# Performance work log

Hardware: AMD Instinct MI355X
Metric: run time of the kernel (lower is better)

Reference implementation:

```python
import jax, jax.numpy as jnp
import numpy as np


def setup_inputs() -> dict:
    key = jax.random.key(0)
    k1, k2 = jax.random.split(key)
    B, EMB, CODES, NUM_TOKENS = 16, 64, 16384, 1024
    x_in = jax.random.normal(k1, (B, EMB, CODES), dtype=jnp.float32)
    code_embedding = jax.random.uniform(k2, (NUM_TOKENS, EMB), dtype=jnp.float32)
    return {"x_in": x_in, "code_embedding": code_embedding}


def reference(x_in, code_embedding):
    # x_in: [B, emb, codes]; code_embedding: [num_tokens, emb]
    x_t = jnp.transpose(x_in, (0, 2, 1))  # [B, codes, emb]
    # squared euclidean distances (argmin is invariant to sqrt used by cdist)
    x2 = jnp.sum(x_t * x_t, axis=-1)                      # [B, codes]
    e2 = jnp.sum(code_embedding * code_embedding, axis=-1)  # [num_tokens]
    dots = jnp.einsum('bce,ke->bck', x_t, code_embedding)   # [B, codes, num_tokens]
    dist2 = x2[:, :, None] - 2.0 * dots + e2[None, None, :]
    indices = jnp.argmin(dist2, axis=2)                   # [B, codes]
    x_out = jnp.transpose(code_embedding[indices], (0, 2, 1))  # [B, emb, codes]
    return x_out, indices[:, :, None]  # indices keepdim like torch argmin(keepdim=True)
```

## Files before the change

### kernel.cpp

```cpp
#include <hip/hip_runtime.h>


#define BB 16
#define EMB 64
#define CODES 16384
#define NT 1024
#define NTILES 64
#define CHUNK 4
#define EPOCHS (NTILES / CHUNK)
#define QPB 256

typedef __attribute__((ext_vector_type(8))) short s16x8;
typedef __attribute__((ext_vector_type(4))) float f32x4;
typedef __attribute__((ext_vector_type(4))) int i32x4;
typedef unsigned int u32;

__device__ inline short bf16_hi(float f) { return (short)(__builtin_bit_cast(u32, f) >> 16); }
__device__ inline float hi_part(float f) { return __builtin_bit_cast(float, __builtin_bit_cast(u32, f) & 0xFFFF0000u); }
__device__ inline u32 umax_(u32 a, u32 b) { return a > b ? a : b; }

__device__ inline void async_copy16(const char* g, char* lds_base_uniform) {
  __builtin_amdgcn_global_load_lds(
      (const __attribute__((address_space(1))) unsigned int*)g,
      (__attribute__((address_space(3))) unsigned int*)(unsigned int)(unsigned long long)lds_base_uniform,
      16, 0, 0);
}

#define WSE_OFF   0
#define WSH_OFF   266240
#define WSH2_OFF  270336

__global__ __launch_bounds__(256) void vq_prep(const float* __restrict__ E,
                                               char* __restrict__ wsE,
                                               float* __restrict__ wsh,
                                               float* __restrict__ wsh2) {
  const int bid = blockIdx.x, tid = threadIdx.x;
  if (bid < 32) {
    const int gid = bid * 256 + tid;
    const int nt = gid >> 7, ks = (gid >> 6) & 1, lane = gid & 63;
    const int col = lane & 15, quad = lane >> 4;
    const int n = nt * 16 + col;
    const int k0 = ks * 32 + quad * 8;
    const float* ep = E + n * EMB + k0;
    s16x8 hv, lv;
    #pragma unroll
    for (int j = 0; j < 8; ++j) {
      float v = ep[j];
      float hf = hi_part(v);
      hv[j] = bf16_hi(v);
      lv[j] = bf16_hi(v - hf);
    }
    char* base = wsE + ((size_t)nt << 12) + ((size_t)ks << 10) + lane * 16;
    *(i32x4*)(base)        = __builtin_bit_cast(i32x4, hv);
    *(i32x4*)(base + 2048) = __builtin_bit_cast(i32x4, lv);
  } else {
    const int n = (bid - 32) * 256 + tid;
    if (n < NT) {
      const float4* ep = (const float4*)(E + n * EMB);
      float s = 0.f;
      #pragma unroll
      for (int g = 0; g < 16; ++g) { float4 v = ep[g]; s += v.x*v.x + v.y*v.y + v.z*v.z + v.w*v.w; }
      const float h = -0.5f * s;
      wsh[n] = h;
      wsh2[n] = 16384.f * (h + 128.f);
    }
  }
}

__global__ __launch_bounds__(512, 4) void vq_main(
    const float* __restrict__ x, const float* __restrict__ E,
    const char* __restrict__ wsE, const float* __restrict__ wsh,
    const float* __restrict__ wsh2,
    float* __restrict__ xout, float* __restrict__ iout) {
  __shared__ char smem[2 * CHUNK * 4096 + 4096];
  float* lh = (float*)(smem + 2 * CHUNK * 4096);
  const int tid = threadIdx.x;
  const int wave = tid >> 6, lane = tid & 63;
  const int col = lane & 15, quad = lane >> 4;
  const int b = blockIdx.y;
  const int c0 = blockIdx.x * QPB;
  const int cw = c0 + wave * 32;

  ((float2*)lh)[tid] = ((const float2*)wsh2)[tid];
  {
    const char* g = wsE + wave * 2048 + lane * 16;
    char* lb = smem + wave * 2048;
    async_copy16(g,        lb);
    async_copy16(g + 1024, lb + 1024);
  }

  s16x8 ah[2][2], al[2][2];
  #pragma unroll
  for (int mt = 0; mt < 2; ++mt) {
    #pragma unroll
    for (int ks = 0; ks < 2; ++ks) {
      s16x8 hv, lv;
      #pragma unroll
      for (int j = 0; j < 8; ++j) {
        const int e = ks * 32 + quad * 8 + j;
        float v = x[((size_t)b * EMB + e) * CODES + (size_t)(cw + mt * 16 + col)] * 16384.f;
        float hf = hi_part(v);
        hv[j] = bf16_hi(v);
        lv[j] = bf16_hi(v - hf);
      }
      ah[mt][ks] = hv;
      al[mt][ks] = lv;
    }
  }

  u32 k1[2][4], k2[2][4];
  #pragma unroll
  for (int mt = 0; mt < 2; ++mt)
    #pragma unroll
    for (int r = 0; r < 4; ++r) { k1[mt][r] = 0u; k2[mt][r] = 0u; }

  u32 inv = 1023u - (u32)col;

  __syncthreads();

  for (int c = 0; c < EPOCHS; ++c) {
    if (c < EPOCHS - 1) {
      const char* g = wsE + (size_t)(c + 1) * (CHUNK * 4096) + wave * 2048 + lane * 16;
      char* lb = smem + ((c + 1) & 1) * (CHUNK * 4096) + wave * 2048;
      async_copy16(g,        lb);
      async_copy16(g + 1024, lb + 1024);
    }

    const char* rb = smem + (c & 1) * (CHUNK * 4096) + lane * 16;
    #pragma unroll
    for (int t = 0; t < CHUNK; ++t) {
      const char* p = rb + t * 4096;
      const s16x8 bh0 = __builtin_bit_cast(s16x8, *(const i32x4*)(p));
      const s16x8 bh1 = __builtin_bit_cast(s16x8, *(const i32x4*)(p + 1024));
      const s16x8 bl0 = __builtin_bit_cast(s16x8, *(const i32x4*)(p + 2048));
      const s16x8 bl1 = __builtin_bit_cast(s16x8, *(const i32x4*)(p + 3072));
      const float ch = lh[(c * CHUNK + t) * 16 + col];
      const f32x4 cq = (f32x4){ch, ch, ch, ch};

      f32x4 acc[2];
      #pragma unroll
      for (int mt = 0; mt < 2; ++mt) {
        acc[mt] = __builtin_amdgcn_mfma_f32_16x16x32_bf16(ah[mt][0], bh0, cq, 0, 0, 0);
        acc[mt] = __builtin_amdgcn_mfma_f32_16x16x32_bf16(ah[mt][1], bh1, acc[mt], 0, 0, 0);
        acc[mt] = __builtin_amdgcn_mfma_f32_16x16x32_bf16(al[mt][0], bh0, acc[mt], 0, 0, 0);
        acc[mt] = __builtin_amdgcn_mfma_f32_16x16x32_bf16(al[mt][1], bh1, acc[mt], 0, 0, 0);
        acc[mt] = __builtin_amdgcn_mfma_f32_16x16x32_bf16(ah[mt][0], bl0, acc[mt], 0, 0, 0);
        acc[mt] = __builtin_amdgcn_mfma_f32_16x16x32_bf16(ah[mt][1], bl1, acc[mt], 0, 0, 0);
      }

      #pragma unroll
      for (int mt = 0; mt < 2; ++mt) {
        #pragma unroll
        for (int r = 0; r < 4; ++r) {
          u32 q = (u32)acc[mt][r];
          u32 key = (q << 10) + inv;
          u32 k1o = k1[mt][r];
          asm("v_med3_u32 %0, %1, %2, %3"
              : "=v"(k2[mt][r]) : "v"(key), "v"(k1o), "v"(k2[mt][r]));
          k1[mt][r] = umax_(key, k1o);
        }
      }
      inv -= 16u;
    }
    __syncthreads();
  }

  uint2* cand = (uint2*)smem;
  int* idxs = (int*)(smem + 2048);
  #pragma unroll
  for (int mt = 0; mt < 2; ++mt) {
    #pragma unroll
    for (int r = 0; r < 4; ++r) {
      u32 a1 = k1[mt][r], a2 = k2[mt][r];
      #pragma unroll
      for (int m = 1; m <= 8; m <<= 1) {
        u32 r1 = __shfl_xor(a1, m, 64);
        u32 r2 = __shfl_xor(a2, m, 64);
        u32 t = a1 < r1 ? a1 : r1;
        a1 = umax_(a1, r1);
        a2 = umax_(umax_(a2, r2), t);
      }
      if (col == r) cand[wave * 32 + mt * 16 + quad * 4 + r] = make_uint2(a1, a2);
    }
  }
  __syncthreads();

  if (tid < QPB) {
    const u32 K1 = cand[tid].x, K2 = cand[tid].y;
    const int i1 = 1023 - (int)(K1 & 1023u);
    const int i2 = 1023 - (int)(K2 & 1023u);
    const float* xq = x + (size_t)b * EMB * CODES + (size_t)(c0 + tid);
    const float4* e1 = (const float4*)(E + i1 * EMB);
    const float4* e2 = (const float4*)(E + i2 * EMB);
    float d10 = 0, d11 = 0, d12 = 0, d13 = 0, d20 = 0, d21 = 0, d22 = 0, d23 = 0;
    #pragma unroll
    for (int g = 0; g < 16; ++g) {
      float4 a = e1[g], c4 = e2[g];
      float x0 = xq[(size_t)(4 * g + 0) * CODES];
      float x1 = xq[(size_t)(4 * g + 1) * CODES];
      float x2 = xq[(size_t)(4 * g + 2) * CODES];
      float x3 = xq[(size_t)(4 * g + 3) * CODES];
      d10 = fmaf(x0, a.x, d10);  d11 = fmaf(x1, a.y, d11);
      d12 = fmaf(x2, a.z, d12);  d13 = fmaf(x3, a.w, d13);
      d20 = fmaf(x0, c4.x, d20); d21 = fmaf(x1, c4.y, d21);
      d22 = fmaf(x2, c4.z, d22); d23 = fmaf(x3, c4.w, d23);
    }
    const float s1 = ((d10 + d11) + (d12 + d13)) + wsh[i1];
    const float s2 = ((d20 + d21) + (d22 + d23)) + wsh[i2];
    const bool take2 = (s2 > s1) || (s2 == s1 && i2 < i1);
    const int idx = take2 ? i2 : i1;
    idxs[tid] = idx;
    iout[(size_t)b * CODES + (size_t)(c0 + tid)] = (float)idx;
  }
  __syncthreads();

  {
    const int q = tid & (QPB - 1);
    const int eh = (tid >> 8) * 32;
    const int idx = idxs[q];
    const float* Er = E + idx * EMB + eh;
    float* xo = xout + ((size_t)b * EMB + eh) * CODES + (size_t)(c0 + q);
    #pragma unroll
    for (int e = 0; e < 32; ++e) xo[(size_t)e * CODES] = Er[e];
  }
}

extern "C" void kernel_launch(void* const* d_in, const int* in_sizes, int n_in,
                              void* d_out, int out_size, void* d_ws, size_t ws_size,
                              hipStream_t stream) {
  const float* x = (const float*)d_in[0];
  const float* E = (const float*)d_in[1];
  float* xout = (float*)d_out;
  float* iout = (float*)d_out + (size_t)BB * EMB * CODES;

  char* wsE  = (char*)d_ws + WSE_OFF;
  float* wsh  = (float*)((char*)d_ws + WSH_OFF);
  float* wsh2 = (float*)((char*)d_ws + WSH2_OFF);

  vq_prep<<<36, 256, 0, stream>>>(E, wsE, wsh, wsh2);
  vq_main<<<dim3(CODES / QPB, BB), 512, 0, stream>>>(x, E, wsE, wsh, wsh2, xout, iout);
}
```

Before: 204.7 us.

## Double CHUNK, prefetch next LDS tile, split MFMA chains, parallelize rescoring

```diff
diff --git a/kernel.cpp b/kernel.cpp
--- a/kernel.cpp
+++ b/kernel.cpp
@@ -6,7 +6,7 @@
 #define CODES 16384
 #define NT 1024
 #define NTILES 64
-#define CHUNK 4
+#define CHUNK 8
 #define EPOCHS (NTILES / CHUNK)
 #define QPB 256
 
@@ -83,10 +83,12 @@
 
   ((float2*)lh)[tid] = ((const float2*)wsh2)[tid];
   {
-    const char* g = wsE + wave * 2048 + lane * 16;
-    char* lb = smem + wave * 2048;
+    const char* g = wsE + wave * 4096 + lane * 16;
+    char* lb = smem + wave * 4096;
     async_copy16(g,        lb);
     async_copy16(g + 1024, lb + 1024);
+    async_copy16(g + 2048, lb + 2048);
+    async_copy16(g + 3072, lb + 3072);
   }
 
   s16x8 ah[2][2], al[2][2];
@@ -120,39 +122,52 @@
 
   for (int c = 0; c < EPOCHS; ++c) {
     if (c < EPOCHS - 1) {
-      const char* g = wsE + (size_t)(c + 1) * (CHUNK * 4096) + wave * 2048 + lane * 16;
-      char* lb = smem + ((c + 1) & 1) * (CHUNK * 4096) + wave * 2048;
+      const char* g = wsE + (size_t)(c + 1) * (CHUNK * 4096) + wave * 4096 + lane * 16;
+      char* lb = smem + ((c + 1) & 1) * (CHUNK * 4096) + wave * 4096;
       async_copy16(g,        lb);
       async_copy16(g + 1024, lb + 1024);
+      async_copy16(g + 2048, lb + 2048);
+      async_copy16(g + 3072, lb + 3072);
     }
 
     const char* rb = smem + (c & 1) * (CHUNK * 4096) + lane * 16;
+    i32x4 fb0 = *(const i32x4*)(rb);
+    i32x4 fb1 = *(const i32x4*)(rb + 1024);
+    i32x4 fb2 = *(const i32x4*)(rb + 2048);
+    i32x4 fb3 = *(const i32x4*)(rb + 3072);
+    float ch = lh[(c * CHUNK) * 16 + col];
+
     #pragma unroll
     for (int t = 0; t < CHUNK; ++t) {
-      const char* p = rb + t * 4096;
-      const s16x8 bh0 = __builtin_bit_cast(s16x8, *(const i32x4*)(p));
-      const s16x8 bh1 = __builtin_bit_cast(s16x8, *(const i32x4*)(p + 1024));
-      const s16x8 bl0 = __builtin_bit_cast(s16x8, *(const i32x4*)(p + 2048));
-      const s16x8 bl1 = __builtin_bit_cast(s16x8, *(const i32x4*)(p + 3072));
-      const float ch = lh[(c * CHUNK + t) * 16 + col];
+      i32x4 nb0, nb1, nb2, nb3; float nch;
+      if (t < CHUNK - 1) {
+        const char* p = rb + (t + 1) * 4096;
+        nb0 = *(const i32x4*)(p);
+        nb1 = *(const i32x4*)(p + 1024);
+        nb2 = *(const i32x4*)(p + 2048);
+        nb3 = *(const i32x4*)(p + 3072);
+        nch = lh[(c * CHUNK + t + 1) * 16 + col];
+      }
+      const s16x8 bh0 = __builtin_bit_cast(s16x8, fb0);
+      const s16x8 bh1 = __builtin_bit_cast(s16x8, fb1);
+      const s16x8 bl0 = __builtin_bit_cast(s16x8, fb2);
+      const s16x8 bl1 = __builtin_bit_cast(s16x8, fb3);
       const f32x4 cq = (f32x4){ch, ch, ch, ch};
-
-      f32x4 acc[2];
+      const f32x4 zz = (f32x4){0.f, 0.f, 0.f, 0.f};
+
       #pragma unroll
       for (int mt = 0; mt < 2; ++mt) {
-        acc[mt] = __builtin_amdgcn_mfma_f32_16x16x32_bf16(ah[mt][0], bh0, cq, 0, 0, 0);
-        acc[mt] = __builtin_amdgcn_mfma_f32_16x16x32_bf16(ah[mt][1], bh1, acc[mt], 0, 0, 0);
-        acc[mt] = __builtin_amdgcn_mfma_f32_16x16x32_bf16(al[mt][0], bh0, acc[mt], 0, 0, 0);
-        acc[mt] = __builtin_amdgcn_mfma_f32_16x16x32_bf16(al[mt][1], bh1, acc[mt], 0, 0, 0);
-        acc[mt] = __builtin_amdgcn_mfma_f32_16x16x32_bf16(ah[mt][0], bl0, acc[mt], 0, 0, 0);
-        acc[mt] = __builtin_amdgcn_mfma_f32_16x16x32_bf16(ah[mt][1], bl1, acc[mt], 0, 0, 0);
-      }
-
-      #pragma unroll
-      for (int mt = 0; mt < 2; ++mt) {
+        f32x4 cA = __builtin_amdgcn_mfma_f32_16x16x32_bf16(ah[mt][0], bh0, cq, 0, 0, 0);
+        f32x4 cB = __builtin_amdgcn_mfma_f32_16x16x32_bf16(al[mt][1], bh1, zz, 0, 0, 0);
+        cA = __builtin_amdgcn_mfma_f32_16x16x32_bf16(ah[mt][1], bh1, cA, 0, 0, 0);
+        cB = __builtin_amdgcn_mfma_f32_16x16x32_bf16(ah[mt][0], bl0, cB, 0, 0, 0);
+        cA = __builtin_amdgcn_mfma_f32_16x16x32_bf16(al[mt][0], bh0, cA, 0, 0, 0);
+        cB = __builtin_amdgcn_mfma_f32_16x16x32_bf16(ah[mt][1], bl1, cB, 0, 0, 0);
+        const f32x4 a = cA + cB;
+
         #pragma unroll
         for (int r = 0; r < 4; ++r) {
-          u32 q = (u32)acc[mt][r];
+          u32 q = (u32)a[r];
           u32 key = (q << 10) + inv;
           u32 k1o = k1[mt][r];
           asm("v_med3_u32 %0, %1, %2, %3"
@@ -161,6 +176,7 @@
         }
       }
       inv -= 16u;
+      if (t < CHUNK - 1) { fb0 = nb0; fb1 = nb1; fb2 = nb2; fb3 = nb3; ch = nch; }
     }
     __syncthreads();
   }
@@ -185,32 +201,30 @@
   }
   __syncthreads();
 
-  if (tid < QPB) {
-    const u32 K1 = cand[tid].x, K2 = cand[tid].y;
-    const int i1 = 1023 - (int)(K1 & 1023u);
-    const int i2 = 1023 - (int)(K2 & 1023u);
-    const float* xq = x + (size_t)b * EMB * CODES + (size_t)(c0 + tid);
-    const float4* e1 = (const float4*)(E + i1 * EMB);
-    const float4* e2 = (const float4*)(E + i2 * EMB);
-    float d10 = 0, d11 = 0, d12 = 0, d13 = 0, d20 = 0, d21 = 0, d22 = 0, d23 = 0;
+  {
+    const int q = tid >> 1, which = tid & 1;
+    const u32 K = which ? cand[q].y : cand[q].x;
+    const int i = 1023 - (int)(K & 1023u);
+    const float* xq = x + (size_t)b * EMB * CODES + (size_t)(c0 + q);
+    const float4* ei = (const float4*)(E + i * EMB);
+    float d0 = 0, d1 = 0, d2 = 0, d3 = 0;
     #pragma unroll
     for (int g = 0; g < 16; ++g) {
-      float4 a = e1[g], c4 = e2[g];
-      float x0 = xq[(size_t)(4 * g + 0) * CODES];
-      float x1 = xq[(size_t)(4 * g + 1) * CODES];
-      float x2 = xq[(size_t)(4 * g + 2) * CODES];
-      float x3 = xq[(size_t)(4 * g + 3) * CODES];
-      d10 = fmaf(x0, a.x, d10);  d11 = fmaf(x1, a.y, d11);
-      d12 = fmaf(x2, a.z, d12);  d13 = fmaf(x3, a.w, d13);
-      d20 = fmaf(x0, c4.x, d20); d21 = fmaf(x1, c4.y, d21);
-      d22 = fmaf(x2, c4.z, d22); d23 = fmaf(x3, c4.w, d23);
-    }
-    const float s1 = ((d10 + d11) + (d12 + d13)) + wsh[i1];
-    const float s2 = ((d20 + d21) + (d22 + d23)) + wsh[i2];
-    const bool take2 = (s2 > s1) || (s2 == s1 && i2 < i1);
-    const int idx = take2 ? i2 : i1;
-    idxs[tid] = idx;
-    iout[(size_t)b * CODES + (size_t)(c0 + tid)] = (float)idx;
+      float4 a = ei[g];
+      d0 = fmaf(xq[(size_t)(4 * g + 0) * CODES], a.x, d0);
+      d1 = fmaf(xq[(size_t)(4 * g + 1) * CODES], a.y, d1);
+      d2 = fmaf(xq[(size_t)(4 * g + 2) * CODES], a.z, d2);
+      d3 = fmaf(xq[(size_t)(4 * g + 3) * CODES], a.w, d3);
+    }
+    const float s = ((d0 + d1) + (d2 + d3)) + wsh[i];
+    const float s_o = __shfl_xor(s, 1, 64);
+    const int i_o = __shfl_xor(i, 1, 64);
+    if (which == 0) {
+      const bool take2 = (s_o > s) || (s_o == s && i_o < i);
+      const int idx = take2 ? i_o : i;
+      idxs[q] = idx;
+      iout[(size_t)b * CODES + (size_t)(c0 + q)] = (float)idx;
+    }
   }
   __syncthreads();
 
```

Result: no change. 208.5 us (+1.8%).

## Switch distance GEMM to 32x32x16 MFMA with 256-thread blocks

Applied to the files above, without the earlier changes.

```diff
diff --git a/kernel.cpp b/kernel.cpp
--- a/kernel.cpp
+++ b/kernel.cpp
@@ -5,13 +5,14 @@
 #define EMB 64
 #define CODES 16384
 #define NT 1024
-#define NTILES 64
+#define NTILES 32
 #define CHUNK 4
 #define EPOCHS (NTILES / CHUNK)
 #define QPB 256
+#define TILE_B 8192
 
 typedef __attribute__((ext_vector_type(8))) short s16x8;
-typedef __attribute__((ext_vector_type(4))) float f32x4;
+typedef __attribute__((ext_vector_type(16))) float f32x16;
 typedef __attribute__((ext_vector_type(4))) int i32x4;
 typedef unsigned int u32;
 
@@ -37,11 +38,8 @@
   const int bid = blockIdx.x, tid = threadIdx.x;
   if (bid < 32) {
     const int gid = bid * 256 + tid;
-    const int nt = gid >> 7, ks = (gid >> 6) & 1, lane = gid & 63;
-    const int col = lane & 15, quad = lane >> 4;
-    const int n = nt * 16 + col;
-    const int k0 = ks * 32 + quad * 8;
-    const float* ep = E + n * EMB + k0;
+    const int n = gid >> 3, ks = (gid >> 1) & 3, half = gid & 1;
+    const float* ep = E + n * EMB + ks * 16 + half * 8;
     s16x8 hv, lv;
     #pragma unroll
     for (int j = 0; j < 8; ++j) {
@@ -50,9 +48,10 @@
       hv[j] = bf16_hi(v);
       lv[j] = bf16_hi(v - hf);
     }
-    char* base = wsE + ((size_t)nt << 12) + ((size_t)ks << 10) + lane * 16;
+    char* base = wsE + ((size_t)(n >> 5)) * TILE_B + (size_t)ks * 1024 +
+                 (size_t)(half * 32 + (n & 31)) * 16;
     *(i32x4*)(base)        = __builtin_bit_cast(i32x4, hv);
-    *(i32x4*)(base + 2048) = __builtin_bit_cast(i32x4, lv);
+    *(i32x4*)(base + 4096) = __builtin_bit_cast(i32x4, lv);
   } else {
     const int n = (bid - 32) * 256 + tid;
     if (n < NT) {
@@ -67,38 +66,53 @@
   }
 }
 
-__global__ __launch_bounds__(512, 4) void vq_main(
+#define MFMA32 __builtin_amdgcn_mfma_f32_32x32x16_bf16
+
+#define TOP2(AV, MT)                                                        \
+  do {                                                                      \
+    _Pragma("unroll")                                                       \
+    for (int r = 0; r < 16; ++r) {                                          \
+      u32 q = (u32)AV[r];                        \
+      u32 key = (q << 10) + inv;                                            \
+      u32 k1o = k1[MT][r];                                                  \
+      asm("v_med3_u32 %0, %1, %2, %3"                                       \
+          : "=v"(k2[MT][r]) : "v"(key), "v"(k1o), "v"(k2[MT][r]));          \
+      k1[MT][r] = umax_(key, k1o);                                          \
+    }                                                                       \
+  } while (0)
+
+__global__ __launch_bounds__(256, 2) void vq_main(
     const float* __restrict__ x, const float* __restrict__ E,
     const char* __restrict__ wsE, const float* __restrict__ wsh,
     const float* __restrict__ wsh2,
     float* __restrict__ xout, float* __restrict__ iout) {
-  __shared__ char smem[2 * CHUNK * 4096 + 4096];
-  float* lh = (float*)(smem + 2 * CHUNK * 4096);
+  __shared__ char smem[2 * CHUNK * TILE_B + 4096];
+  float* lh = (float*)(smem + 2 * CHUNK * TILE_B);
   const int tid = threadIdx.x;
   const int wave = tid >> 6, lane = tid & 63;
-  const int col = lane & 15, quad = lane >> 4;
+  const int col = lane & 31, half = lane >> 5;
   const int b = blockIdx.y;
   const int c0 = blockIdx.x * QPB;
-  const int cw = c0 + wave * 32;
-
-  ((float2*)lh)[tid] = ((const float2*)wsh2)[tid];
+  const int cw = c0 + wave * 64;
+
+  ((float4*)lh)[tid] = ((const float4*)wsh2)[tid];
   {
-    const char* g = wsE + wave * 2048 + lane * 16;
-    char* lb = smem + wave * 2048;
-    async_copy16(g,        lb);
-    async_copy16(g + 1024, lb + 1024);
-  }
-
-  s16x8 ah[2][2], al[2][2];
+    const char* g = wsE + wave * TILE_B + lane * 16;
+    char* lb = smem + wave * TILE_B;
+    #pragma unroll
+    for (int i = 0; i < 8; ++i) async_copy16(g + i * 1024, lb + i * 1024);
+  }
+
+  s16x8 ah[2][4], al[2][4];
   #pragma unroll
   for (int mt = 0; mt < 2; ++mt) {
     #pragma unroll
-    for (int ks = 0; ks < 2; ++ks) {
+    for (int ks = 0; ks < 4; ++ks) {
       s16x8 hv, lv;
       #pragma unroll
       for (int j = 0; j < 8; ++j) {
-        const int e = ks * 32 + quad * 8 + j;
-        float v = x[((size_t)b * EMB + e) * CODES + (size_t)(cw + mt * 16 + col)] * 16384.f;
+        const int e = ks * 16 + half * 8 + j;
+        float v = x[((size_t)b * EMB + e) * CODES + (size_t)(cw + mt * 32 + col)] * 16384.f;
         float hf = hi_part(v);
         hv[j] = bf16_hi(v);
         lv[j] = bf16_hi(v - hf);
@@ -108,11 +122,11 @@
     }
   }
 
-  u32 k1[2][4], k2[2][4];
+  u32 k1[2][16], k2[2][16];
   #pragma unroll
   for (int mt = 0; mt < 2; ++mt)
     #pragma unroll
-    for (int r = 0; r < 4; ++r) { k1[mt][r] = 0u; k2[mt][r] = 0u; }
+    for (int r = 0; r < 16; ++r) { k1[mt][r] = 0u; k2[mt][r] = 0u; }
 
   u32 inv = 1023u - (u32)col;
 
@@ -120,47 +134,46 @@
 
   for (int c = 0; c < EPOCHS; ++c) {
     if (c < EPOCHS - 1) {
-      const char* g = wsE + (size_t)(c + 1) * (CHUNK * 4096) + wave * 2048 + lane * 16;
-      char* lb = smem + ((c + 1) & 1) * (CHUNK * 4096) + wave * 2048;
-      async_copy16(g,        lb);
-      async_copy16(g + 1024, lb + 1024);
-    }
-
-    const char* rb = smem + (c & 1) * (CHUNK * 4096) + lane * 16;
+      const char* g = wsE + (size_t)(c + 1) * (CHUNK * TILE_B) + wave * TILE_B + lane * 16;
+      char* lb = smem + ((c + 1) & 1) * (CHUNK * TILE_B) + wave * TILE_B;
+      #pragma unroll
+      for (int i = 0; i < 8; ++i) async_copy16(g + i * 1024, lb + i * 1024);
+    }
+
+    const char* rb = smem + (c & 1) * (CHUNK * TILE_B) + lane * 16;
     #pragma unroll
     for (int t = 0; t < CHUNK; ++t) {
-      const char* p = rb + t * 4096;
+      const char* p = rb + t * TILE_B;
       const s16x8 bh0 = __builtin_bit_cast(s16x8, *(const i32x4*)(p));
       const s16x8 bh1 = __builtin_bit_cast(s16x8, *(const i32x4*)(p + 1024));
-      const s16x8 bl0 = __builtin_bit_cast(s16x8, *(const i32x4*)(p + 2048));
-      const s16x8 bl1 = __builtin_bit_cast(s16x8, *(const i32x4*)(p + 3072));
-      const float ch = lh[(c * CHUNK + t) * 16 + col];
-      const f32x4 cq = (f32x4){ch, ch, ch, ch};
-
-      f32x4 acc[2];
-      #pragma unroll
-      for (int mt = 0; mt < 2; ++mt) {
-        acc[mt] = __builtin_amdgcn_mfma_f32_16x16x32_bf16(ah[mt][0], bh0, cq, 0, 0, 0);
-        acc[mt] = __builtin_amdgcn_mfma_f32_16x16x32_bf16(ah[mt][1], bh1, acc[mt], 0, 0, 0);
-        acc[mt] = __builtin_amdgcn_mfma_f32_16x16x32_bf16(al[mt][0], bh0, acc[mt], 0, 0, 0);
-        acc[mt] = __builtin_amdgcn_mfma_f32_16x16x32_bf16(al[mt][1], bh1, acc[mt], 0, 0, 0);
-        acc[mt] = __builtin_amdgcn_mfma_f32_16x16x32_bf16(ah[mt][0], bl0, acc[mt], 0, 0, 0);
-        acc[mt] = __builtin_amdgcn_mfma_f32_16x16x32_bf16(ah[mt][1], bl1, acc[mt], 0, 0, 0);
-      }
-
-      #pragma unroll
-      for (int mt = 0; mt < 2; ++mt) {
-        #pragma unroll
-        for (int r = 0; r < 4; ++r) {
-          u32 q = (u32)acc[mt][r];
-          u32 key = (q << 10) + inv;
-          u32 k1o = k1[mt][r];
-          asm("v_med3_u32 %0, %1, %2, %3"
-              : "=v"(k2[mt][r]) : "v"(key), "v"(k1o), "v"(k2[mt][r]));
-          k1[mt][r] = umax_(key, k1o);
-        }
-      }
-      inv -= 16u;
+      const s16x8 bh2 = __builtin_bit_cast(s16x8, *(const i32x4*)(p + 2048));
+      const s16x8 bh3 = __builtin_bit_cast(s16x8, *(const i32x4*)(p + 3072));
+      const s16x8 bl0 = __builtin_bit_cast(s16x8, *(const i32x4*)(p + 4096));
+      const s16x8 bl1 = __builtin_bit_cast(s16x8, *(const i32x4*)(p + 5120));
+      const s16x8 bl2 = __builtin_bit_cast(s16x8, *(const i32x4*)(p + 6144));
+      const s16x8 bl3 = __builtin_bit_cast(s16x8, *(const i32x4*)(p + 7168));
+      const float ch = lh[(c * CHUNK + t) * 32 + col];
+
+      f32x16 a0, a1;
+      #pragma unroll
+      for (int i = 0; i < 16; ++i) { a0[i] = ch; a1[i] = ch; }
+
+      a0 = MFMA32(ah[0][0], bh0, a0, 0, 0, 0);  a1 = MFMA32(ah[1][0], bh0, a1, 0, 0, 0);
+      a0 = MFMA32(ah[0][1], bh1, a0, 0, 0, 0);  a1 = MFMA32(ah[1][1], bh1, a1, 0, 0, 0);
+      a0 = MFMA32(ah[0][2], bh2, a0, 0, 0, 0);  a1 = MFMA32(ah[1][2], bh2, a1, 0, 0, 0);
+      a0 = MFMA32(ah[0][3], bh3, a0, 0, 0, 0);  a1 = MFMA32(ah[1][3], bh3, a1, 0, 0, 0);
+      a0 = MFMA32(al[0][0], bh0, a0, 0, 0, 0);  a1 = MFMA32(al[1][0], bh0, a1, 0, 0, 0);
+      a0 = MFMA32(al[0][1], bh1, a0, 0, 0, 0);  a1 = MFMA32(al[1][1], bh1, a1, 0, 0, 0);
+      a0 = MFMA32(al[0][2], bh2, a0, 0, 0, 0);  a1 = MFMA32(al[1][2], bh2, a1, 0, 0, 0);
+      a0 = MFMA32(al[0][3], bh3, a0, 0, 0, 0);  a1 = MFMA32(al[1][3], bh3, a1, 0, 0, 0);
+      a0 = MFMA32(ah[0][0], bl0, a0, 0, 0, 0);  a1 = MFMA32(ah[1][0], bl0, a1, 0, 0, 0);
+      a0 = MFMA32(ah[0][1], bl1, a0, 0, 0, 0);  a1 = MFMA32(ah[1][1], bl1, a1, 0, 0, 0);
+      a0 = MFMA32(ah[0][2], bl2, a0, 0, 0, 0);  a1 = MFMA32(ah[1][2], bl2, a1, 0, 0, 0);
+      a0 = MFMA32(ah[0][3], bl3, a0, 0, 0, 0);  a1 = MFMA32(ah[1][3], bl3, a1, 0, 0, 0);
+
+      TOP2(a0, 0);
+      TOP2(a1, 1);
+      inv -= 32u;
     }
     __syncthreads();
   }
@@ -170,22 +183,24 @@
   #pragma unroll
   for (int mt = 0; mt < 2; ++mt) {
     #pragma unroll
-    for (int r = 0; r < 4; ++r) {
-      u32 a1 = k1[mt][r], a2 = k2[mt][r];
-      #pragma unroll
-      for (int m = 1; m <= 8; m <<= 1) {
-        u32 r1 = __shfl_xor(a1, m, 64);
-        u32 r2 = __shfl_xor(a2, m, 64);
-        u32 t = a1 < r1 ? a1 : r1;
-        a1 = umax_(a1, r1);
-        a2 = umax_(umax_(a2, r2), t);
+    for (int r = 0; r < 16; ++r) {
+      u32 a1k = k1[mt][r], a2k = k2[mt][r];
+      #pragma unroll
+      for (int m = 1; m <= 16; m <<= 1) {
+        u32 r1 = __shfl_xor(a1k, m, 64);
+        u32 r2 = __shfl_xor(a2k, m, 64);
+        u32 t = a1k < r1 ? a1k : r1;
+        a1k = umax_(a1k, r1);
+        a2k = umax_(umax_(a2k, r2), t);
       }
-      if (col == r) cand[wave * 32 + mt * 16 + quad * 4 + r] = make_uint2(a1, a2);
+      if (col == r)
+        cand[wave * 64 + mt * 32 + (r & 3) + 8 * (r >> 2) + 4 * half] =
+            make_uint2(a1k, a2k);
     }
   }
   __syncthreads();
 
-  if (tid < QPB) {
+  {
     const u32 K1 = cand[tid].x, K2 = cand[tid].y;
     const int i1 = 1023 - (int)(K1 & 1023u);
     const int i2 = 1023 - (int)(K2 & 1023u);
@@ -215,13 +230,11 @@
   __syncthreads();
 
   {
-    const int q = tid & (QPB - 1);
-    const int eh = (tid >> 8) * 32;
-    const int idx = idxs[q];
-    const float* Er = E + idx * EMB + eh;
-    float* xo = xout + ((size_t)b * EMB + eh) * CODES + (size_t)(c0 + q);
-    #pragma unroll
-    for (int e = 0; e < 32; ++e) xo[(size_t)e * CODES] = Er[e];
+    const int idx = idxs[tid];
+    const float* Er = E + idx * EMB;
+    float* xo = xout + (size_t)b * EMB * CODES + (size_t)(c0 + tid);
+    #pragma unroll
+    for (int e = 0; e < EMB; ++e) xo[(size_t)e * CODES] = Er[e];
   }
 }
 
@@ -238,5 +251,5 @@
   float* wsh2 = (float*)((char*)d_ws + WSH2_OFF);
 
   vq_prep<<<36, 256, 0, stream>>>(E, wsE, wsh, wsh2);
-  vq_main<<<dim3(CODES / QPB, BB), 512, 0, stream>>>(x, E, wsE, wsh, wsh2, xout, iout);
-}
+  vq_main<<<dim3(CODES / QPB, BB), 256, 0, stream>>>(x, E, wsE, wsh, wsh2, xout, iout);
+}
```

After: 212.7 us. +3.9%, slower.
